# Kernel optimization log

Hardware: AMD Instinct MI355X
Metric: run time of the kernel (lower is better)

Reference implementation:

```python
import jax, jax.numpy as jnp
import numpy as np

H, B, C, T, F = 4, 2, 64, 2048, 64   # n_head, batch, in_chan, time, n_freqs
HID = 4                               # hid_chan (per-head Q/K channels)
VD = C // H                           # per-head V channels
EPS = 1e-5


def prelu(x, a):
    return jnp.where(x >= 0, x, a * x)


def ln_cf(x, g, b):
    # LayerNormalization4D: normalize over (channel, freq) axes of (..., C, T, F)
    mu = x.mean(axis=(-3, -1), keepdims=True)
    var = ((x - mu) ** 2).mean(axis=(-3, -1), keepdims=True)
    return (x - mu) / jnp.sqrt(var + EPS) * g + b


def setup_inputs() -> dict:
    key = jax.random.key(0)
    ks = jax.random.split(key, 8)

    def w(k, shape):
        return jax.random.normal(k, shape, jnp.float32) * 0.05

    return {
        "x": jax.random.normal(ks[0], (B, C, T, F), jnp.float32),
        # per-head 1x1-conv Q/K/V projections (stacked over head axis)
        "Wq": w(ks[1], (H, HID, C)), "bq": jnp.zeros((H, HID), jnp.float32),
        "aq": jnp.full((H,), 0.25, jnp.float32),
        "gq": jnp.ones((H, HID, F), jnp.float32), "betq": jnp.zeros((H, HID, F), jnp.float32),
        "Wk": w(ks[2], (H, HID, C)), "bk": jnp.zeros((H, HID), jnp.float32),
        "ak": jnp.full((H,), 0.25, jnp.float32),
        "gk": jnp.ones((H, HID, F), jnp.float32), "betk": jnp.zeros((H, HID, F), jnp.float32),
        "Wv": w(ks[3], (H, VD, C)), "bv": jnp.zeros((H, VD), jnp.float32),
        "av": jnp.full((H,), 0.25, jnp.float32),
        "gv": jnp.ones((H, VD, F), jnp.float32), "betv": jnp.zeros((H, VD, F), jnp.float32),
        # output 1x1-conv projection
        "Wp": w(ks[4], (C, C)), "bp": jnp.zeros((C,), jnp.float32),
        "ap": jnp.full((), 0.25, jnp.float32),
        "gp": jnp.ones((C, F), jnp.float32), "betp": jnp.zeros((C, F), jnp.float32),
    }


def reference(x, Wq, bq, aq, gq, betq, Wk, bk, ak, gk, betk,
              Wv, bv, av, gv, betv, Wp, bp, ap, gp, betp):
    def qkv(W, b, a, g, be):
        # batched per-head 1x1 conv: (H,O,C) x (B,C,T,F) -> (H,B,O,T,F)
        y = jnp.einsum('hoc,bctf->hbotf', W, x) + b[:, None, :, None, None]
        y = prelu(y, a[:, None, None, None, None])
        return ln_cf(y, g[:, None, :, None, :], be[:, None, :, None, :])

    Q = qkv(Wq, bq, aq, gq, betq).reshape(H * B, HID, T, F)
    K = qkv(Wk, bk, ak, gk, betk).reshape(H * B, HID, T, F)
    V = qkv(Wv, bv, av, gv, betv).reshape(H * B, VD, T, F)

    # (HB, C', T, F) -> (HB, T, C'*F)
    Q = Q.transpose(0, 2, 1, 3).reshape(H * B, T, HID * F)
    K = K.transpose(0, 2, 1, 3).reshape(H * B, T, HID * F)
    V = V.transpose(0, 2, 1, 3).reshape(H * B, T, VD * F)

    scale = 1.0 / jnp.sqrt(jnp.asarray(HID * F, jnp.float32))
    attn = jax.nn.softmax(jnp.einsum('bqd,bkd->bqk', Q, K) * scale, axis=-1)  # (HB,T,T)
    O = jnp.einsum('bqk,bkd->bqd', attn, V)                                    # (HB,T,VD*F)

    # (HB,T,VD,F) -> (B, H*VD, T, F) matching torch head-concat order
    O = O.reshape(H * B, T, VD, F).transpose(0, 2, 1, 3)
    O = O.reshape(H, B, VD, T, F).transpose(1, 0, 2, 3, 4).reshape(B, H * VD, T, F)

    y = jnp.einsum('oc,bctf->botf', Wp, O) + bp[None, :, None, None]
    y = prelu(y, ap)
    y = ln_cf(y, gp[:, None, :], betp[:, None, :])
    return y + x
```

## Files before the change

### kernel.cpp

```cpp
#include <hip/hip_runtime.h>

#define EPS_ 1e-5f

typedef float f32x4 __attribute__((ext_vector_type(4)));
typedef short s16x8 __attribute__((ext_vector_type(8)));

static __device__ __forceinline__ short f2bf(float f) {
    unsigned u = __float_as_uint(f);
    unsigned r = (u + 0x7FFFu + ((u >> 16) & 1u)) >> 16;
    return (short)r;
}
static __device__ __forceinline__ float bf2f(short s) {
    return __uint_as_float(((unsigned)(unsigned short)s) << 16);
}

static __device__ __forceinline__ void gload16(const short* g, short* l) {
    __builtin_amdgcn_global_load_lds(
        (const __attribute__((address_space(1))) unsigned int*)g,
        (__attribute__((address_space(3))) unsigned int*)l, 16, 0, 0);
}

__global__ __launch_bounds__(256) void prep_kernel(
    const float* __restrict__ Wq, const float* __restrict__ Wk,
    const float* __restrict__ Wv, const float* __restrict__ Wp,
    short* __restrict__ Wbf, short* __restrict__ Wpbf)
{
    int i = blockIdx.x * 256 + threadIdx.x;
    if (i < 6144) {
        float v = (i < 1024) ? Wq[i] : (i < 2048 ? Wk[i - 1024] : Wv[i - 2048]);
        Wbf[i] = f2bf(v);
    } else if (i < 6144 + 4096) {
        Wpbf[i - 6144] = f2bf(Wp[i - 6144]);
    }
}

__global__ __launch_bounds__(256) void qkv_kernel(
    const float* __restrict__ x, const short* __restrict__ Wbf,
    const float* __restrict__ bq, const float* __restrict__ aq,
    const float* __restrict__ gq, const float* __restrict__ betq,
    const float* __restrict__ bk, const float* __restrict__ ak,
    const float* __restrict__ gk, const float* __restrict__ betk,
    const float* __restrict__ bv, const float* __restrict__ av,
    const float* __restrict__ gv, const float* __restrict__ betv,
    short* __restrict__ Qo, short* __restrict__ Ko, short* __restrict__ Vo)
{
    const int t = blockIdx.x;
    const int b = blockIdx.y;
    const int tid = threadIdx.x;
    const int wid = tid >> 6, lane = tid & 63;
    const int g = lane >> 4, c16 = lane & 15;
    const int f_ = tid & 63, cg = tid >> 6;

    __shared__ __align__(16) short wlds[96 * 64];
    __shared__ __align__(16) short xs[64 * 64];
    __shared__ float zs[96 * 64];
    __shared__ float stats[12][2];
    __shared__ float bias_l[96], alpha_l[96];

#pragma unroll
    for (int j = 0; j < 3; ++j) {
        int i8 = tid + 256 * j;
        int row = i8 >> 3, cb = i8 & 7;
        s16x8 v = *(const s16x8*)(Wbf + i8 * 8);
        *(s16x8*)&wlds[row * 64 + ((cb ^ (row & 7)) * 8)] = v;
    }
    if (tid < 96) {
        int row = tid; float bias, al;
        if (row < 16)      { bias = bq[row];      al = aq[row >> 2]; }
        else if (row < 32) { bias = bk[row - 16]; al = ak[(row - 16) >> 2]; }
        else               { bias = bv[row - 32]; al = av[(row - 32) >> 4]; }
        bias_l[row] = bias; alpha_l[row] = al;
    }
#pragma unroll
    for (int it = 0; it < 2; ++it) {
        int cb = cg + 4 * it, c0 = cb * 8;
        s16x8 v;
#pragma unroll
        for (int i = 0; i < 8; ++i)
            v[i] = f2bf(x[(((size_t)b * 64 + c0 + i) * 2048 + t) * 64 + f_]);
        *(s16x8*)&xs[f_ * 64 + ((cb ^ (f_ & 7)) * 8)] = v;
    }
    __syncthreads();

    const int f0 = wid * 16;
    s16x8 bfr[2];
#pragma unroll
    for (int kk = 0; kk < 2; ++kk)
        bfr[kk] = *(const s16x8*)&xs[(f0 + c16) * 64 + (((kk * 4 + g) ^ (c16 & 7)) * 8)];

    f32x4 acc[6];
#pragma unroll
    for (int rt = 0; rt < 6; ++rt) {
#pragma unroll
        for (int r = 0; r < 4; ++r) acc[rt][r] = 0.f;
#pragma unroll
        for (int kk = 0; kk < 2; ++kk) {
            s16x8 a = *(const s16x8*)&wlds[(rt * 16 + c16) * 64 + (((kk * 4 + g) ^ (c16 & 7)) * 8)];
            acc[rt] = __builtin_amdgcn_mfma_f32_16x16x32_bf16(a, bfr[kk], acc[rt], 0, 0, 0);
        }
    }

#pragma unroll
    for (int rt = 0; rt < 6; ++rt)
#pragma unroll
        for (int r = 0; r < 4; ++r) {
            int row = rt * 16 + g * 4 + r;
            float z = acc[rt][r] + bias_l[row];
            z = z >= 0.f ? z : alpha_l[row] * z;
            zs[row * 64 + f0 + c16] = z;
        }
    __syncthreads();

#pragma unroll
    for (int gi = 0; gi < 3; ++gi) {
        int grp = wid * 3 + gi;
        int base_row, n;
        if (grp < 4)      { base_row = grp * 4;             n = 256; }
        else if (grp < 8) { base_row = 16 + (grp - 4) * 4;  n = 256; }
        else              { base_row = 32 + (grp - 8) * 16; n = 1024; }
        int cnt = n >> 6;
        float s = 0.f, ss = 0.f;
        for (int i = 0; i < cnt; ++i) {
            float v = zs[(base_row + i) * 64 + lane];
            s += v; ss += v * v;
        }
#pragma unroll
        for (int msk = 32; msk >= 1; msk >>= 1) {
            s  += __shfl_xor(s, msk);
            ss += __shfl_xor(ss, msk);
        }
        if (lane == 0) {
            float mean = s / n;
            float var = ss / n - mean * mean;
            stats[grp][0] = mean;
            stats[grp][1] = rsqrtf(var + EPS_);
        }
    }
    __syncthreads();

#pragma unroll
    for (int j = 0; j < 24; ++j) {
        int row = cg + 4 * j;
        float zv = zs[row * 64 + f_];
        if (row < 16) {
            int grp = row >> 2;
            float val = (zv - stats[grp][0]) * stats[grp][1];
            val = val * gq[row * 64 + f_] + betq[row * 64 + f_];
            int h = row >> 2, o = row & 3;
            Qo[(((size_t)(h * 2 + b)) * 2048 + t) * 256 + o * 64 + f_] = f2bf(val);
        } else if (row < 32) {
            int rr = row - 16, grp = 4 + (rr >> 2);
            float val = (zv - stats[grp][0]) * stats[grp][1];
            val = val * gk[rr * 64 + f_] + betk[rr * 64 + f_];
            int h = rr >> 2, o = rr & 3;
            Ko[(((size_t)(h * 2 + b)) * 2048 + t) * 256 + o * 64 + f_] = f2bf(val);
        } else {
            int rr = row - 32, grp = 8 + (rr >> 4);
            float val = (zv - stats[grp][0]) * stats[grp][1];
            val = val * gv[rr * 64 + f_] + betv[rr * 64 + f_];
            int h = rr >> 4, ov = rr & 15;
            Vo[(((size_t)(h * 2 + b)) * 2048 + t) * 1024 + ov * 64 + f_] = f2bf(val);
        }
    }
}

__global__ __launch_bounds__(256) void vtrans_kernel(
    const short* __restrict__ Vrm, short* __restrict__ Vt)
{
    const int t0 = blockIdx.x * 64;
    const int d0 = blockIdx.y * 64;
    const int hb = blockIdx.z;
    const int tid = threadIdx.x;
    __shared__ __align__(16) short tile[64 * 72];

#pragma unroll
    for (int k = 0; k < 2; ++k) {
        int q = tid + 256 * k;
        int row = q >> 3, slot = q & 7;
        s16x8 v = *(const s16x8*)(Vrm + ((size_t)hb * 2048 + t0 + row) * 1024 + d0 + slot * 8);
        *(s16x8*)&tile[row * 72 + slot * 8] = v;
    }
    __syncthreads();
#pragma unroll
    for (int k = 0; k < 2; ++k) {
        int q = tid + 256 * k;
        int drow = q >> 3, tslot = q & 7;
        s16x8 v;
#pragma unroll
        for (int i = 0; i < 8; ++i)
            v[i] = tile[(tslot * 8 + i) * 72 + drow];
        *(s16x8*)(Vt + ((size_t)hb * 1024 + d0 + drow) * 2048 + t0 + tslot * 8) = v;
    }
}

__global__ __launch_bounds__(512, 2) void attn_kernel(
    const short* __restrict__ Qg, const short* __restrict__ Kg,
    const short* __restrict__ Vt, short* __restrict__ Ob)
{
    const int hb = blockIdx.x;
    const int qt = blockIdx.y;
    const int t0 = qt * 64;
    const int tid = threadIdx.x;
    const int lane = tid & 63;
    const int wid = tid >> 6;
    const int qs = wid >> 1;
    const int kp = wid & 1;
    const int g = lane >> 4, c16 = lane & 15;

    __shared__ __align__(16) short k_lds[2][64 * 256];
    __shared__ __align__(16) short p_lds[2][64 * 68];
    __shared__ float lpart[2][64];

    const size_t qbase = ((size_t)hb * 2048 + t0 + qs * 16 + c16) * 256;
    const int dsl = wid * 128;
    const size_t vrow0 = (size_t)hb * 1024 + dsl + c16;
    const size_t kgbase = (size_t)hb * 2048 * 256;

    f32x4 oacc[32];
#pragma unroll
    for (int i = 0; i < 32; ++i)
#pragma unroll
        for (int r = 0; r < 4; ++r) oacc[i][r] = 0.f;

    float l_r[4] = {0.f, 0.f, 0.f, 0.f};

#define STAGE_K(buf, kt) do {                                                  \
    _Pragma("unroll")                                                          \
    for (int j_ = 0; j_ < 4; ++j_) {                                           \
        int c_ = (wid * 4 + j_) * 64 + lane;                                   \
        int row_ = c_ >> 5, sp_ = c_ & 31;                                     \
        int slot_ = sp_ ^ (row_ & 7);                                          \
        gload16(Kg + kgbase + (size_t)((kt) * 64 + row_) * 256 + slot_ * 8,    \
                &k_lds[buf][(wid * 4 + j_) * 512]);                            \
    }                                                                          \
} while (0)

#define QKT_PHASE(nt) do {                                                     \
    s16x8 qf[8];                                                               \
    _Pragma("unroll")                                                          \
    for (int kf = 0; kf < 8; ++kf)                                             \
        qf[kf] = *(const s16x8*)(Qg + qbase + kf * 32 + g * 8);                \
    f32x4 sf[2];                                                               \
    _Pragma("unroll")                                                          \
    for (int nf = 0; nf < 2; ++nf)                                             \
        _Pragma("unroll")                                                      \
        for (int r = 0; r < 4; ++r) sf[nf][r] = 0.f;                           \
    __builtin_amdgcn_s_setprio(1);                                             \
    _Pragma("unroll")                                                          \
    for (int kf = 0; kf < 8; ++kf) {                                           \
        _Pragma("unroll")                                                      \
        for (int nf = 0; nf < 2; ++nf) {                                       \
            int krow = kp * 32 + nf * 16 + c16;                                \
            s16x8 kb = *(const s16x8*)&k_lds[(nt) & 1]                         \
                [krow * 256 + (((kf * 4 + g) ^ (krow & 7)) * 8)];              \
            sf[nf] = __builtin_amdgcn_mfma_f32_16x16x32_bf16(qf[kf], kb, sf[nf], 0, 0, 0); \
        }                                                                      \
    }                                                                          \
    __builtin_amdgcn_s_setprio(0);                                             \
    float rs[4] = {0.f, 0.f, 0.f, 0.f};                                        \
    _Pragma("unroll")                                                          \
    for (int nf = 0; nf < 2; ++nf)                                             \
        _Pragma("unroll")                                                      \
        for (int r = 0; r < 4; ++r) {                                          \
            float p = __expf(sf[nf][r] * 0.0625f);                             \
            sf[nf][r] = p;                                                     \
            rs[r] += p;                                                        \
        }                                                                      \
    _Pragma("unroll")                                                          \
    for (int msk = 1; msk <= 8; msk <<= 1)                                     \
        _Pragma("unroll")                                                      \
        for (int r = 0; r < 4; ++r) rs[r] += __shfl_xor(rs[r], msk);           \
    _Pragma("unroll")                                                          \
    for (int r = 0; r < 4; ++r) l_r[r] += rs[r];                               \
    _Pragma("unroll")                                                          \
    for (int nf = 0; nf < 2; ++nf)                                             \
        _Pragma("unroll")                                                      \
        for (int r = 0; r < 4; ++r)                                            \
            p_lds[(nt) & 1][(qs * 16 + g * 4 + r) * 68 + kp * 32 + nf * 16 + c16] \
                = f2bf(sf[nf][r]);                                             \
} while (0)

    STAGE_K(0, 0);
    __syncthreads();
    STAGE_K(1, 1);
    QKT_PHASE(0);
    __syncthreads();

    for (int t = 0; t < 32; ++t) {
        const int kt0 = t * 64;

        s16x8 vf[2][2];
#pragma unroll
        for (int dt = 0; dt < 2; ++dt)
#pragma unroll
            for (int ks = 0; ks < 2; ++ks)
                vf[dt][ks] = *(const s16x8*)(Vt + (vrow0 + dt * 16) * 2048 + kt0 + (ks * 4 + g) * 8);

        if (t < 30) STAGE_K(t & 1, t + 2);
        if (t < 31) QKT_PHASE(t + 1);

        s16x8 pa[4][2];
#pragma unroll
        for (int s4 = 0; s4 < 4; ++s4)
#pragma unroll
            for (int ks = 0; ks < 2; ++ks)
                pa[s4][ks] = *(const s16x8*)&p_lds[t & 1][(s4 * 16 + c16) * 68 + ks * 32 + g * 8];

#pragma unroll
        for (int dt = 0; dt < 8; ++dt) {
            __builtin_amdgcn_s_setprio(1);
#pragma unroll
            for (int s4 = 0; s4 < 4; ++s4)
#pragma unroll
                for (int ks = 0; ks < 2; ++ks)
                    oacc[dt * 4 + s4] = __builtin_amdgcn_mfma_f32_16x16x32_bf16(
                        pa[s4][ks], vf[dt & 1][ks], oacc[dt * 4 + s4], 0, 0, 0);
            __builtin_amdgcn_s_setprio(0);
            if (dt < 6) {
#pragma unroll
                for (int ks = 0; ks < 2; ++ks)
                    vf[dt & 1][ks] = *(const s16x8*)(Vt + (vrow0 + (dt + 2) * 16) * 2048 + kt0 + (ks * 4 + g) * 8);
            }
        }

        if (t < 31) __syncthreads();
    }

#undef STAGE_K
#undef QKT_PHASE

    __syncthreads();
    if (c16 == 0) {
#pragma unroll
        for (int r = 0; r < 4; ++r)
            lpart[kp][qs * 16 + g * 4 + r] = l_r[r];
    }
    __syncthreads();

    float li[16];
#pragma unroll
    for (int s4 = 0; s4 < 4; ++s4)
#pragma unroll
        for (int r = 0; r < 4; ++r) {
            int row = s4 * 16 + g * 4 + r;
            li[s4 * 4 + r] = 1.f / (lpart[0][row] + lpart[1][row]);
        }

    const int h = hb >> 1, b = hb & 1;
#pragma unroll
    for (int dt = 0; dt < 8; ++dt) {
        int vcol = dsl + dt * 16 + c16;
        int cout = h * 16 + (vcol >> 6), ff = vcol & 63;
#pragma unroll
        for (int s4 = 0; s4 < 4; ++s4)
#pragma unroll
            for (int r = 0; r < 4; ++r) {
                int trow = t0 + s4 * 16 + g * 4 + r;
                Ob[(((size_t)b * 64 + cout) * 2048 + trow) * 64 + ff] =
                    f2bf(oacc[dt * 4 + s4][r] * li[s4 * 4 + r]);
            }
    }
}

__global__ __launch_bounds__(256) void oproj_kernel(
    const short* __restrict__ Ob, const float* __restrict__ x,
    const short* __restrict__ Wpbf,
    const float* __restrict__ bp, const float* __restrict__ ap,
    const float* __restrict__ gp, const float* __restrict__ betp,
    float* __restrict__ out)
{
    const int t = blockIdx.x;
    const int b = blockIdx.y;
    const int tid = threadIdx.x;
    const int wid = tid >> 6, lane = tid & 63;
    const int g = lane >> 4, c16 = lane & 15;
    const int f_ = tid & 63, cg = tid >> 6;

    __shared__ __align__(16) short wp[64 * 64];
    __shared__ __align__(16) short os[64 * 64];
    __shared__ float zs[64 * 64];
    __shared__ float red[4][2];

#pragma unroll
    for (int j = 0; j < 2; ++j) {
        int i8 = tid + 256 * j;
        int row = i8 >> 3, cb = i8 & 7;
        s16x8 v = *(const s16x8*)(Wpbf + i8 * 8);
        *(s16x8*)&wp[row * 64 + ((cb ^ (row & 7)) * 8)] = v;
    }
#pragma unroll
    for (int it = 0; it < 2; ++it) {
        int cb = cg + 4 * it, c0 = cb * 8;
        s16x8 v;
#pragma unroll
        for (int i = 0; i < 8; ++i)
            v[i] = Ob[(((size_t)b * 64 + c0 + i) * 2048 + t) * 64 + f_];
        *(s16x8*)&os[f_ * 64 + ((cb ^ (f_ & 7)) * 8)] = v;
    }
    __syncthreads();

    const int f0 = wid * 16;
    s16x8 bfr[2];
#pragma unroll
    for (int kk = 0; kk < 2; ++kk)
        bfr[kk] = *(const s16x8*)&os[(f0 + c16) * 64 + (((kk * 4 + g) ^ (c16 & 7)) * 8)];

    const float ap0 = ap[0];
    f32x4 acc[4];
#pragma unroll
    for (int rt = 0; rt < 4; ++rt) {
#pragma unroll
        for (int r = 0; r < 4; ++r) acc[rt][r] = 0.f;
#pragma unroll
        for (int kk = 0; kk < 2; ++kk) {
            s16x8 a = *(const s16x8*)&wp[(rt * 16 + c16) * 64 + (((kk * 4 + g) ^ (c16 & 7)) * 8)];
            acc[rt] = __builtin_amdgcn_mfma_f32_16x16x32_bf16(a, bfr[kk], acc[rt], 0, 0, 0);
        }
    }

#pragma unroll
    for (int rt = 0; rt < 4; ++rt)
#pragma unroll
        for (int r = 0; r < 4; ++r) {
            int row = rt * 16 + g * 4 + r;
            float z = acc[rt][r] + bp[row];
            z = z >= 0.f ? z : ap0 * z;
            zs[row * 64 + f0 + c16] = z;
        }
    __syncthreads();

    float s = 0.f, ss = 0.f;
#pragma unroll
    for (int j = 0; j < 16; ++j) {
        float v = zs[(cg + 4 * j) * 64 + f_];
        s += v; ss += v * v;
    }
#pragma unroll
    for (int msk = 32; msk >= 1; msk >>= 1) {
        s  += __shfl_xor(s, msk);
        ss += __shfl_xor(ss, msk);
    }
    if (lane == 0) { red[wid][0] = s; red[wid][1] = ss; }
    __syncthreads();
    float ts  = red[0][0] + red[1][0] + red[2][0] + red[3][0];
    float tss = red[0][1] + red[1][1] + red[2][1] + red[3][1];
    float mean = ts * (1.f / 4096.f);
    float rstd = rsqrtf(tss * (1.f / 4096.f) - mean * mean + EPS_);

#pragma unroll
    for (int j = 0; j < 16; ++j) {
        int row = cg + 4 * j;
        size_t idx = (((size_t)b * 64 + row) * 2048 + t) * 64 + f_;
        out[idx] = (zs[row * 64 + f_] - mean) * rstd * gp[row * 64 + f_]
                 + betp[row * 64 + f_] + x[idx];
    }
}

extern "C" void kernel_launch(void* const* d_in, const int* in_sizes, int n_in,
                              void* d_out, int out_size, void* d_ws, size_t ws_size,
                              hipStream_t stream)
{
    const float* x    = (const float*)d_in[0];
    const float* Wq   = (const float*)d_in[1];
    const float* bq   = (const float*)d_in[2];
    const float* aq   = (const float*)d_in[3];
    const float* gq   = (const float*)d_in[4];
    const float* betq = (const float*)d_in[5];
    const float* Wk   = (const float*)d_in[6];
    const float* bk   = (const float*)d_in[7];
    const float* ak   = (const float*)d_in[8];
    const float* gk   = (const float*)d_in[9];
    const float* betk = (const float*)d_in[10];
    const float* Wv   = (const float*)d_in[11];
    const float* bv   = (const float*)d_in[12];
    const float* av   = (const float*)d_in[13];
    const float* gv   = (const float*)d_in[14];
    const float* betv = (const float*)d_in[15];
    const float* Wp   = (const float*)d_in[16];
    const float* bp   = (const float*)d_in[17];
    const float* ap   = (const float*)d_in[18];
    const float* gp   = (const float*)d_in[19];
    const float* betp = (const float*)d_in[20];

    short* Qb   = (short*)d_ws;
    short* Kb   = Qb   + (size_t)8 * 2048 * 256;
    short* Vrm  = Kb   + (size_t)8 * 2048 * 256;
    short* Vt   = Vrm  + (size_t)8 * 2048 * 1024;
    short* Obuf = Vt   + (size_t)8 * 2048 * 1024;
    short* Wbf  = Obuf + (size_t)8 * 2048 * 1024;
    short* Wpbf = Wbf  + 96 * 64;

    prep_kernel<<<40, 256, 0, stream>>>(Wq, Wk, Wv, Wp, Wbf, Wpbf);
    qkv_kernel<<<dim3(2048, 2), 256, 0, stream>>>(x, Wbf,
        bq, aq, gq, betq, bk, ak, gk, betk, bv, av, gv, betv, Qb, Kb, Vrm);
    vtrans_kernel<<<dim3(32, 16, 8), 256, 0, stream>>>(Vrm, Vt);
    attn_kernel<<<dim3(8, 32), 512, 0, stream>>>(Qb, Kb, Vt, Obuf);
    oproj_kernel<<<dim3(2048, 2), 256, 0, stream>>>(Obuf, x, Wpbf,
        bp, ap, gp, betp, (float*)d_out);
}
```

Before: 265.1 us.

## Retile attention to 128-query blocks with split V dimension across grid z

Each attention block now handles 128 query rows, with the 1024-wide V dimension split into two halves across blockIdx.z, so every wave owns 16 query rows over the full 64-key tile. Q fragments are loaded once into registers instead of on every key step. Each wave then computes its own full row sums, which removes the cross-wave l partials. QK^T work is duplicated across the two V-half blocks, and the V fragments are loaded up front rather than streamed during the MFMA loop. This is meant to raise V reuse per P tile and cut the repeated Q loads, at the cost of extra QK^T compute and higher register pressure.

```diff
diff --git a/kernel.cpp b/kernel.cpp
--- a/kernel.cpp
+++ b/kernel.cpp
@@ -199,22 +199,26 @@
 {
     const int hb = blockIdx.x;
     const int qt = blockIdx.y;
-    const int t0 = qt * 64;
+    const int dh = blockIdx.z;
+    const int t0 = qt * 128;
     const int tid = threadIdx.x;
     const int lane = tid & 63;
     const int wid = tid >> 6;
-    const int qs = wid >> 1;
-    const int kp = wid & 1;
     const int g = lane >> 4, c16 = lane & 15;
 
     __shared__ __align__(16) short k_lds[2][64 * 256];
-    __shared__ __align__(16) short p_lds[2][64 * 68];
-    __shared__ float lpart[2][64];
-
-    const size_t qbase = ((size_t)hb * 2048 + t0 + qs * 16 + c16) * 256;
-    const int dsl = wid * 128;
+    __shared__ __align__(16) short p_lds[2][128 * 66];
+    __shared__ float l_sh[128];
+
+    const size_t kgbase = (size_t)hb * 2048 * 256;
+    const int dsl = dh * 512 + wid * 64;
     const size_t vrow0 = (size_t)hb * 1024 + dsl + c16;
-    const size_t kgbase = (size_t)hb * 2048 * 256;
+
+    const size_t qbase = ((size_t)hb * 2048 + t0 + wid * 16 + c16) * 256;
+    s16x8 qf[8];
+#pragma unroll
+    for (int kf = 0; kf < 8; ++kf)
+        qf[kf] = *(const s16x8*)(Qg + qbase + kf * 32 + g * 8);
 
     f32x4 oacc[32];
 #pragma unroll
@@ -236,21 +240,17 @@
 } while (0)
 
 #define QKT_PHASE(nt) do {                                                     \
-    s16x8 qf[8];                                                               \
-    _Pragma("unroll")                                                          \
-    for (int kf = 0; kf < 8; ++kf)                                             \
-        qf[kf] = *(const s16x8*)(Qg + qbase + kf * 32 + g * 8);                \
-    f32x4 sf[2];                                                               \
-    _Pragma("unroll")                                                          \
-    for (int nf = 0; nf < 2; ++nf)                                             \
+    f32x4 sf[4];                                                               \
+    _Pragma("unroll")                                                          \
+    for (int nf = 0; nf < 4; ++nf)                                             \
         _Pragma("unroll")                                                      \
         for (int r = 0; r < 4; ++r) sf[nf][r] = 0.f;                           \
     __builtin_amdgcn_s_setprio(1);                                             \
     _Pragma("unroll")                                                          \
     for (int kf = 0; kf < 8; ++kf) {                                           \
         _Pragma("unroll")                                                      \
-        for (int nf = 0; nf < 2; ++nf) {                                       \
-            int krow = kp * 32 + nf * 16 + c16;                                \
+        for (int nf = 0; nf < 4; ++nf) {                                       \
+            int krow = nf * 16 + c16;                                          \
             s16x8 kb = *(const s16x8*)&k_lds[(nt) & 1]                         \
                 [krow * 256 + (((kf * 4 + g) ^ (krow & 7)) * 8)];              \
             sf[nf] = __builtin_amdgcn_mfma_f32_16x16x32_bf16(qf[kf], kb, sf[nf], 0, 0, 0); \
@@ -259,7 +259,7 @@
     __builtin_amdgcn_s_setprio(0);                                             \
     float rs[4] = {0.f, 0.f, 0.f, 0.f};                                        \
     _Pragma("unroll")                                                          \
-    for (int nf = 0; nf < 2; ++nf)                                             \
+    for (int nf = 0; nf < 4; ++nf)                                             \
         _Pragma("unroll")                                                      \
         for (int r = 0; r < 4; ++r) {                                          \
             float p = __expf(sf[nf][r] * 0.0625f);                             \
@@ -273,10 +273,10 @@
     _Pragma("unroll")                                                          \
     for (int r = 0; r < 4; ++r) l_r[r] += rs[r];                               \
     _Pragma("unroll")                                                          \
-    for (int nf = 0; nf < 2; ++nf)                                             \
+    for (int nf = 0; nf < 4; ++nf)                                             \
         _Pragma("unroll")                                                      \
         for (int r = 0; r < 4; ++r)                                            \
-            p_lds[(nt) & 1][(qs * 16 + g * 4 + r) * 68 + kp * 32 + nf * 16 + c16] \
+            p_lds[(nt) & 1][(wid * 16 + g * 4 + r) * 66 + nf * 16 + c16]       \
                 = f2bf(sf[nf][r]);                                             \
 } while (0)
 
@@ -289,9 +289,9 @@
     for (int t = 0; t < 32; ++t) {
         const int kt0 = t * 64;
 
-        s16x8 vf[2][2];
-#pragma unroll
-        for (int dt = 0; dt < 2; ++dt)
+        s16x8 vf[4][2];
+#pragma unroll
+        for (int dt = 0; dt < 4; ++dt)
 #pragma unroll
             for (int ks = 0; ks < 2; ++ks)
                 vf[dt][ks] = *(const s16x8*)(Vt + (vrow0 + dt * 16) * 2048 + kt0 + (ks * 4 + g) * 8);
@@ -299,28 +299,25 @@
         if (t < 30) STAGE_K(t & 1, t + 2);
         if (t < 31) QKT_PHASE(t + 1);
 
-        s16x8 pa[4][2];
-#pragma unroll
-        for (int s4 = 0; s4 < 4; ++s4)
-#pragma unroll
-            for (int ks = 0; ks < 2; ++ks)
-                pa[s4][ks] = *(const s16x8*)&p_lds[t & 1][(s4 * 16 + c16) * 68 + ks * 32 + g * 8];
-
-#pragma unroll
-        for (int dt = 0; dt < 8; ++dt) {
+#pragma unroll
+        for (int h2 = 0; h2 < 2; ++h2) {
+            s16x8 pa[4][2];
+#pragma unroll
+            for (int qs = 0; qs < 4; ++qs)
+#pragma unroll
+                for (int ks = 0; ks < 2; ++ks)
+                    pa[qs][ks] = *(const s16x8*)&p_lds[t & 1]
+                        [((h2 * 4 + qs) * 16 + c16) * 66 + ks * 32 + g * 8];
             __builtin_amdgcn_s_setprio(1);
 #pragma unroll
-            for (int s4 = 0; s4 < 4; ++s4)
-#pragma unroll
-                for (int ks = 0; ks < 2; ++ks)
-                    oacc[dt * 4 + s4] = __builtin_amdgcn_mfma_f32_16x16x32_bf16(
-                        pa[s4][ks], vf[dt & 1][ks], oacc[dt * 4 + s4], 0, 0, 0);
+            for (int qs = 0; qs < 4; ++qs)
+#pragma unroll
+                for (int dt = 0; dt < 4; ++dt)
+#pragma unroll
+                    for (int ks = 0; ks < 2; ++ks)
+                        oacc[(h2 * 4 + qs) * 4 + dt] = __builtin_amdgcn_mfma_f32_16x16x32_bf16(
+                            pa[qs][ks], vf[dt][ks], oacc[(h2 * 4 + qs) * 4 + dt], 0, 0, 0);
             __builtin_amdgcn_s_setprio(0);
-            if (dt < 6) {
-#pragma unroll
-                for (int ks = 0; ks < 2; ++ks)
-                    vf[dt & 1][ks] = *(const s16x8*)(Vt + (vrow0 + (dt + 2) * 16) * 2048 + kt0 + (ks * 4 + g) * 8);
-            }
         }
 
         if (t < 31) __syncthreads();
@@ -333,32 +330,25 @@
     if (c16 == 0) {
 #pragma unroll
         for (int r = 0; r < 4; ++r)
-            lpart[kp][qs * 16 + g * 4 + r] = l_r[r];
-    }
-    __syncthreads();
-
-    float li[16];
-#pragma unroll
-    for (int s4 = 0; s4 < 4; ++s4)
-#pragma unroll
-        for (int r = 0; r < 4; ++r) {
-            int row = s4 * 16 + g * 4 + r;
-            li[s4 * 4 + r] = 1.f / (lpart[0][row] + lpart[1][row]);
-        }
+            l_sh[wid * 16 + g * 4 + r] = l_r[r];
+    }
+    __syncthreads();
 
     const int h = hb >> 1, b = hb & 1;
 #pragma unroll
-    for (int dt = 0; dt < 8; ++dt) {
-        int vcol = dsl + dt * 16 + c16;
-        int cout = h * 16 + (vcol >> 6), ff = vcol & 63;
-#pragma unroll
-        for (int s4 = 0; s4 < 4; ++s4)
+    for (int qs2 = 0; qs2 < 8; ++qs2) {
+#pragma unroll
+        for (int dt = 0; dt < 4; ++dt) {
+            int vcol = dsl + dt * 16 + c16;
+            int cout = h * 16 + (vcol >> 6), ff = vcol & 63;
 #pragma unroll
             for (int r = 0; r < 4; ++r) {
-                int trow = t0 + s4 * 16 + g * 4 + r;
+                int trow = t0 + qs2 * 16 + g * 4 + r;
+                float li = 1.f / l_sh[qs2 * 16 + g * 4 + r];
                 Ob[(((size_t)b * 64 + cout) * 2048 + trow) * 64 + ff] =
-                    f2bf(oacc[dt * 4 + s4][r] * li[s4 * 4 + r]);
+                    f2bf(oacc[qs2 * 4 + dt][r] * li);
             }
+        }
     }
 }
 
@@ -494,7 +484,7 @@
     qkv_kernel<<<dim3(2048, 2), 256, 0, stream>>>(x, Wbf,
         bq, aq, gq, betq, bk, ak, gk, betk, bv, av, gv, betv, Qb, Kb, Vrm);
     vtrans_kernel<<<dim3(32, 16, 8), 256, 0, stream>>>(Vrm, Vt);
-    attn_kernel<<<dim3(8, 32), 512, 0, stream>>>(Qb, Kb, Vt, Obuf);
+    attn_kernel<<<dim3(8, 16, 2), 512, 0, stream>>>(Qb, Kb, Vt, Obuf);
     oproj_kernel<<<dim3(2048, 2), 256, 0, stream>>>(Obuf, x, Wpbf,
         bp, ap, gp, betp, (float*)d_out);
 }
```

Measured after the change: 310.1 us. 1.17x slower.
